# Optimization experiments

Measured on AMD Instinct MI355X. Metric: run time of the kernel, lower is better.

Reference implementation:

```python
import jax, jax.numpy as jnp
import numpy as np

# dims: D=embed_dim (= number of experts), H=heads, P=image patches, Q=query embeddings, B=batch
D, H, N, P, B, Q = 256, 8, 256, 1024, 1, 64
HD = D // H
EPS = 1e-5


def _ln(x, g, b):
    m = x.mean(-1, keepdims=True)
    v = x.var(-1, keepdims=True)
    return (x - m) / jnp.sqrt(v + EPS) * g + b


def _mha(q_x, kv_x, Wqkv, bqkv, Wo, bo):
    # standard torch nn.MultiheadAttention (batch_first, eval mode)
    Wq, Wk, Wv = jnp.split(Wqkv, 3, axis=0)
    bq, bk, bv = jnp.split(bqkv, 3, axis=0)
    q = q_x @ Wq.T + bq
    k = kv_x @ Wk.T + bk
    v = kv_x @ Wv.T + bv
    Bq, S, _ = q.shape
    Sk = k.shape[1]
    qh = q.reshape(Bq, S, H, HD)
    kh = k.reshape(Bq, Sk, H, HD)
    vh = v.reshape(Bq, Sk, H, HD)
    att = jax.nn.softmax(jnp.einsum('bqhd,bkhd->bhqk', qh, kh) / np.sqrt(HD).astype(np.float32), axis=-1)
    ctx = jnp.einsum('bhqk,bkhd->bqhd', att, vh).reshape(Bq, S, D)
    return ctx @ Wo.T + bo


def setup_inputs() -> dict:
    key = jax.random.key(0)
    ks = jax.random.split(key, 12)
    s = 0.02  # weight init scale
    return {
        'image_patches': jax.random.normal(ks[0], (B, P, D), jnp.float32),
        'expert_tokens': jax.random.normal(ks[1], (B, N, D), jnp.float32),
        'query_embeddings': jax.random.normal(ks[2], (B, Q, D), jnp.float32),
        'Wqkv_experts': jax.random.normal(ks[3], (N, 3 * D, D), jnp.float32) * s,
        'bqkv_experts': jnp.zeros((N, 3 * D), jnp.float32),
        'Wo_experts': jax.random.normal(ks[4], (N, D, D), jnp.float32) * s,
        'bo_experts': jnp.zeros((N, D), jnp.float32),
        'Wqkv_q': jax.random.normal(ks[5], (3 * D, D), jnp.float32) * s,
        'bqkv_q': jnp.zeros((3 * D,), jnp.float32),
        'Wo_q': jax.random.normal(ks[6], (D, D), jnp.float32) * s,
        'bo_q': jnp.zeros((D,), jnp.float32),
        'Wqkv_s': jax.random.normal(ks[7], (3 * D, D), jnp.float32) * s,
        'bqkv_s': jnp.zeros((3 * D,), jnp.float32),
        'Wo_s': jax.random.normal(ks[8], (D, D), jnp.float32) * s,
        'bo_s': jnp.zeros((D,), jnp.float32),
        'W1': jax.random.normal(ks[9], (4 * D, D), jnp.float32) * s,
        'b1': jnp.zeros((4 * D,), jnp.float32),
        'W2': jax.random.normal(ks[10], (D, 4 * D), jnp.float32) * s,
        'b2': jnp.zeros((D,), jnp.float32),
        'ln1_g': jnp.ones((D,), jnp.float32), 'ln1_b': jnp.zeros((D,), jnp.float32),
        'ln2_g': jnp.ones((D,), jnp.float32), 'ln2_b': jnp.zeros((D,), jnp.float32),
        'ln3_g': jnp.ones((D,), jnp.float32), 'ln3_b': jnp.zeros((D,), jnp.float32),
    }


def reference(image_patches, expert_tokens, query_embeddings,
              Wqkv_experts, bqkv_experts, Wo_experts, bo_experts,
              Wqkv_q, bqkv_q, Wo_q, bo_q,
              Wqkv_s, bqkv_s, Wo_s, bo_s,
              W1, b1, W2, b2,
              ln1_g, ln1_b, ln2_g, ln2_b, ln3_g, ln3_b):
    # --- per-expert cross attention (the embed_dim separate MHA calls, fused/batched) ---
    Wq, Wk, Wv = jnp.split(Wqkv_experts, 3, axis=1)   # each [N, D, D]
    bq, bk, bv = jnp.split(bqkv_experts, 3, axis=1)   # each [N, D]
    q = jnp.einsum('bnd,ned->bne', expert_tokens, Wq) + bq                       # [B,N,D]
    K = jnp.einsum('bpd,ned->bnpe', image_patches, Wk) + bk[None, :, None, :]    # [B,N,P,D]
    V = jnp.einsum('bpd,ned->bnpe', image_patches, Wv) + bv[None, :, None, :]    # [B,N,P,D]
    qh = q.reshape(B, N, H, HD)
    Kh = K.reshape(B, N, P, H, HD)
    Vh = V.reshape(B, N, P, H, HD)
    att = jax.nn.softmax(jnp.einsum('bnhd,bnphd->bnhp', qh, Kh) / np.sqrt(HD).astype(np.float32), axis=-1)
    image_attention_weights = att.mean(axis=2)        # [B,N,P] head-averaged, torch default
    ctx = jnp.einsum('bnhp,bnphd->bnhd', att, Vh).reshape(B, N, D)
    attended_image = jnp.einsum('bnd,ned->bne', ctx, Wo_experts) + bo_experts    # [B,N,D]
    attended_image = _ln(attended_image + expert_tokens, ln1_g, ln1_b)
    # --- query cross attention ---
    attended_query = _mha(attended_image, query_embeddings, Wqkv_q, bqkv_q, Wo_q, bo_q)
    attended_query = _ln(attended_query + attended_image, ln2_g, ln2_b)
    # --- FFN (no residual in original) ---
    expert_refined = jax.nn.relu(attended_query @ W1.T + b1) @ W2.T + b2
    # --- expert self attention + residual + norm ---
    sa = _mha(expert_refined, expert_refined, Wqkv_s, bqkv_s, Wo_s, bo_s)
    expert_features = _ln(sa + expert_refined, ln3_g, ln3_b)
    return expert_features, image_attention_weights
```

## Files before the change

kernel.cpp:

```cpp
#include <hip/hip_runtime.h>

#define DD 256
#define NH 8
#define NP 1024
#define NQ 64
#define SCALE 0.17677669529663687f

typedef float f32x4v __attribute__((ext_vector_type(4)));
typedef __bf16 bfv8 __attribute__((ext_vector_type(8)));

union BF8 { bfv8 v; unsigned short u16[8]; uint4 q; };

__device__ __forceinline__ float wred_sum(float p) {
  #pragma unroll
  for (int m = 32; m; m >>= 1) p += __shfl_xor(p, m);
  return p;
}
__device__ __forceinline__ float wred_max(float p) {
  #pragma unroll
  for (int m = 32; m; m >>= 1) p = fmaxf(p, __shfl_xor(p, m));
  return p;
}
__device__ __forceinline__ float red8(float p) {
  p += __shfl_xor(p, 1);
  p += __shfl_xor(p, 2);
  p += __shfl_xor(p, 4);
  return p;
}
__device__ __forceinline__ float red16(float p) {
  p += __shfl_xor(p, 1);
  p += __shfl_xor(p, 2);
  p += __shfl_xor(p, 4);
  p += __shfl_xor(p, 8);
  return p;
}
__device__ __forceinline__ float dot4(float4 a, float4 b) {
  return a.x*b.x + a.y*b.y + a.z*b.z + a.w*b.w;
}
__device__ __forceinline__ unsigned short f2b(float f) {
  unsigned int u = __float_as_uint(f);
  u += 0x7fffu + ((u >> 16) & 1u);
  return (unsigned short)(u >> 16);
}
__device__ __forceinline__ BF8 cvt8(float4 a, float4 b) {
  BF8 r;
  r.u16[0]=f2b(a.x); r.u16[1]=f2b(a.y); r.u16[2]=f2b(a.z); r.u16[3]=f2b(a.w);
  r.u16[4]=f2b(b.x); r.u16[5]=f2b(b.y); r.u16[6]=f2b(b.z); r.u16[7]=f2b(b.w);
  return r;
}
__device__ __forceinline__ f32x4v mfma16(BF8 a, BF8 b, f32x4v c) {
  return __builtin_amdgcn_mfma_f32_16x16x32_bf16(a.v, b.v, c, 0, 0, 0);
}
__device__ __forceinline__ float2 b2f2(unsigned int u) {
  return make_float2(__uint_as_float(u << 16), __uint_as_float(u & 0xffff0000u));
}
__device__ __forceinline__ float dotb8(uint4 w, float4 x0, float4 x1) {
  float2 p0 = b2f2(w.x), p1 = b2f2(w.y), p2 = b2f2(w.z), p3 = b2f2(w.w);
  return p0.x*x0.x + p0.y*x0.y + p1.x*x0.z + p1.y*x0.w
       + p2.x*x1.x + p2.y*x1.y + p3.x*x1.z + p3.y*x1.w;
}

__device__ __forceinline__ void preload8(const float* x, int lane, float4* xf) {
  const int o = (lane & 7) * 4;
  #pragma unroll
  for (int cc = 0; cc < 8; ++cc) xf[cc] = *(const float4*)&x[cc*32 + o];
}
__device__ __forceinline__ void pass16(const float* __restrict__ W, int ldk,
                                       int r0, int lane, const float4* xf,
                                       float* outA, float* outB) {
  const float* baseA = W + (size_t)(r0 + (lane >> 3))*ldk + (lane & 7)*4;
  const float* baseB = baseA + (size_t)8*ldk;
  float4 wa[8], wb[8];
  #pragma unroll
  for (int cc = 0; cc < 8; ++cc) wa[cc] = *(const float4*)&baseA[cc*32];
  #pragma unroll
  for (int cc = 0; cc < 8; ++cc) wb[cc] = *(const float4*)&baseB[cc*32];
  float a = 0.f, b = 0.f;
  #pragma unroll
  for (int cc = 0; cc < 8; ++cc) { a += dot4(wa[cc], xf[cc]); b += dot4(wb[cc], xf[cc]); }
  *outA = red8(a); *outB = red8(b);
}
__device__ __forceinline__ void preload8b(const float* x, int lane, float4* xf) {
  const int o = (lane & 7) * 8;
  #pragma unroll
  for (int cc = 0; cc < 4; ++cc) {
    xf[2*cc]   = *(const float4*)&x[cc*64 + o];
    xf[2*cc+1] = *(const float4*)&x[cc*64 + o + 4];
  }
}
__device__ __forceinline__ void pass16b(const unsigned short* __restrict__ W, int ldk,
                                        int r0, int lane, const float4* xf,
                                        float* outA, float* outB) {
  const unsigned short* baseA = W + (size_t)(r0 + (lane >> 3))*ldk + (lane & 7)*8;
  const unsigned short* baseB = baseA + (size_t)8*ldk;
  uint4 wa[4], wb[4];
  #pragma unroll
  for (int cc = 0; cc < 4; ++cc) wa[cc] = *(const uint4*)&baseA[cc*64];
  #pragma unroll
  for (int cc = 0; cc < 4; ++cc) wb[cc] = *(const uint4*)&baseB[cc*64];
  float a = 0.f, b = 0.f;
  #pragma unroll
  for (int cc = 0; cc < 4; ++cc) {
    a += dotb8(wa[cc], xf[2*cc], xf[2*cc+1]);
    b += dotb8(wb[cc], xf[2*cc], xf[2*cc+1]);
  }
  *outA = red8(a); *outB = red8(b);
}

__device__ __forceinline__ void layernorm_store(const float* buf, float* outp,
                                                const float* g, const float* b,
                                                float* red, int tid, int wid, int lane)
{
  __syncthreads();
  if (wid == 0) {
    float s = buf[lane] + buf[lane+64] + buf[lane+128] + buf[lane+192];
    s = wred_sum(s);
    if (!lane) red[0] = s * (1.f/256.f);
  }
  __syncthreads();
  float mn = red[0];
  if (wid == 0) {
    float d0 = buf[lane]-mn, d1 = buf[lane+64]-mn, d2 = buf[lane+128]-mn, d3 = buf[lane+192]-mn;
    float s = d0*d0 + d1*d1 + d2*d2 + d3*d3;
    s = wred_sum(s);
    if (!lane) red[1] = rsqrtf(s * (1.f/256.f) + 1e-5f);
  }
  __syncthreads();
  if (tid < 256) outp[tid] = (buf[tid] - mn) * red[1] * g[tid] + b[tid];
}

__device__ __forceinline__ void stage8(const float* __restrict__ Wrow0, float* stf, int lane) {
  #pragma unroll
  for (int r = 0; r < 8; ++r)
    __builtin_amdgcn_global_load_lds(
      (const __attribute__((address_space(1))) unsigned int*)(Wrow0 + (size_t)r*DD + lane*4),
      (__attribute__((address_space(3))) unsigned int*)(stf + r*258), 16, 0, 0);
}
#define WAITV0() { asm volatile("s_waitcnt vmcnt(0)" ::: "memory"); __builtin_amdgcn_sched_barrier(0); }
#define ENDIT()  { asm volatile("s_waitcnt lgkmcnt(0)" ::: "memory"); __builtin_amdgcn_sched_barrier(0); }

__device__ __forceinline__ float rowdot4(const float* stf, int row, int j, const float4* xq) {
  float a = 0.f;
  #pragma unroll
  for (int cc = 0; cc < 4; ++cc) {
    float4 wv = *(const float4*)&stf[row*258 + cc*64 + j*4];
    a += dot4(wv, xq[cc]);
  }
  return red16(a);
}

__global__ __launch_bounds__(256)
void k_pre(const float* __restrict__ patches, uint4* __restrict__ pTB,
           uint4* __restrict__ patchesB,
           const float* __restrict__ qe, const float* __restrict__ Wqkv_q,
           const float* __restrict__ bqkv_q, float* __restrict__ kvq,
           const float* __restrict__ Wo_q, const float* __restrict__ W1,
           const float* __restrict__ W2, const float* __restrict__ Wqkv_s,
           unsigned short* __restrict__ wsB)
{
  const int b = blockIdx.x, tid = threadIdx.x;
  if (b < 128) {
    const int T = b*4 + (tid >> 6), l = tid & 63;
    const int kt = T >> 6, nt = T & 63;
    const int row = nt*16 + (l & 15), col = kt*32 + (l >> 4)*8;
    float4 a = *(const float4*)&patches[(size_t)row*DD + col];
    float4 c = *(const float4*)&patches[(size_t)row*DD + col + 4];
    pTB[(size_t)T*64 + l] = cvt8(a, c).q;
  } else if (b < 256) {
    const int T = (b - 128)*4 + (tid >> 6), l = tid & 63;
    const int kt = T >> 4, nt = T & 15;
    const int col = nt*16 + (l & 15), p0 = kt*32 + (l >> 4)*8;
    float v[8];
    #pragma unroll
    for (int j = 0; j < 8; ++j) v[j] = patches[(size_t)(p0 + j)*DD + col];
    BF8 r;
    #pragma unroll
    for (int j = 0; j < 8; ++j) r.u16[j] = f2b(v[j]);
    patchesB[(size_t)T*64 + l] = r.q;
  } else if (b < 320) {
    __shared__ float x[DD], kvrow[512];
    const int j = b - 256, w = tid >> 6, lane = tid & 63;
    if (tid < DD) x[tid] = qe[j*DD + tid];
    __syncthreads();
    float4 xf[8]; preload8(x, lane, xf);
    #pragma unroll
    for (int g = 0; g < 8; ++g) {
      int r0 = w*128 + g*16;
      float a, bb;
      pass16(Wqkv_q + (size_t)DD*DD, DD, r0, lane, xf, &a, &bb);
      int rA = r0 + (lane >> 3);
      if ((lane & 7) == 0) {
        kvrow[rA]   = a  + bqkv_q[DD + rA];
        kvrow[rA+8] = bb + bqkv_q[DD + rA + 8];
      }
    }
    __syncthreads();
    kvq[(size_t)j*512 + tid]       = kvrow[tid];
    kvq[(size_t)j*512 + 256 + tid] = kvrow[256 + tid];
  } else {
    const int gid = (b - 320)*256 + tid;
    const float* src;
    size_t dof;
    if      (gid < 8192)  { src = Wqkv_q + (size_t)gid*8;           dof = (size_t)gid*8; }
    else if (gid < 16384) { src = Wo_q   + (size_t)(gid-8192)*8;    dof = 65536  + (size_t)(gid-8192)*8; }
    else if (gid < 49152) { src = W1     + (size_t)(gid-16384)*8;   dof = 131072 + (size_t)(gid-16384)*8; }
    else if (gid < 81920) { src = W2     + (size_t)(gid-49152)*8;   dof = 393216 + (size_t)(gid-49152)*8; }
    else                  { src = Wqkv_s + (size_t)(gid-81920)*8;   dof = 655360 + (size_t)(gid-81920)*8; }
    float4 a = *(const float4*)&src[0];
    float4 c = *(const float4*)&src[4];
    *(uint4*)&wsB[dof] = cvt8(a, c).q;
  }
}

__global__ __launch_bounds__(512)
void k_front(const float* __restrict__ et_g,
             const float* __restrict__ Wqkv_e, const float* __restrict__ bqkv_e,
             const float* __restrict__ Wo_e, const float* __restrict__ bo_e,
             const uint4* __restrict__ pTB, const uint4* __restrict__ patchesB,
             const float* __restrict__ ln1g, const float* __restrict__ ln1b,
             float* __restrict__ aln_g, float* __restrict__ iaw)
{
  const int n = blockIdx.x, tid = threadIdx.x, w = tid >> 6, lane = tid & 63;
  __shared__ float stageF[8*8*258];
  __shared__ float attS[NH][NP];
  __shared__ __align__(16) uint4 attB[16][128];
  __shared__ float tS[16][260];
  __shared__ float uS[NH][DD];
  __shared__ float xL[DD], qL[DD], ctxL[DD], resS[DD], red2[2];

  const float* Wn = Wqkv_e + (size_t)n*(3*DD*DD);
  const float* bn = bqkv_e + (size_t)n*(3*DD);
  float* stf = &stageF[w*2064];
  const int j16 = lane & 15, g16 = lane >> 4;

  if (tid < DD) xL[tid] = et_g[(size_t)n*DD + tid];
  __syncthreads();

  {
    float4 xq[4];
    #pragma unroll
    for (int cc = 0; cc < 4; ++cc) xq[cc] = *(const float4*)&xL[j16*4 + cc*64];
    #pragma unroll
    for (int grp = 0; grp < 4; ++grp) {
      stage8(Wn + (size_t)(w*32 + grp*8)*DD, stf, lane);
      WAITV0();
      float a0 = rowdot4(stf, g16,     j16, xq);
      float a1 = rowdot4(stf, 4 + g16, j16, xq);
      if (j16 == 0) {
        qL[w*32 + grp*8 + g16]     = a0;
        qL[w*32 + grp*8 + 4 + g16] = a1;
      }
      ENDIT();
    }
    if (lane < 32) qL[w*32 + lane] += bn[w*32 + lane];
  }

  {
    const float* Wk = Wn + (size_t)DD*DD + (size_t)w*32*DD;
    float4 acc = make_float4(0.f, 0.f, 0.f, 0.f);
    #pragma unroll
    for (int grp = 0; grp < 4; ++grp) {
      stage8(Wk + (size_t)grp*8*DD, stf, lane);
      WAITV0();
      #pragma unroll
      for (int r = 0; r < 8; ++r) {
        float qs = qL[w*32 + grp*8 + r];
        float4 wv = *(const float4*)&stf[r*258 + lane*4];
        acc.x += qs*wv.x; acc.y += qs*wv.y; acc.z += qs*wv.z; acc.w += qs*wv.w;
      }
      ENDIT();
    }
    *(float4*)&tS[w][4*lane] = acc;
  }
  __syncthreads();

  BF8 afr[8];
  {
    const int rr = lane & 15, ko = (lane >> 4)*8;
    #pragma unroll
    for (int kt = 0; kt < 8; ++kt) {
      float4 a = *(const float4*)&tS[rr][kt*32 + ko];
      float4 c = *(const float4*)&tS[rr][kt*32 + ko + 4];
      afr[kt] = cvt8(a, c);
    }
  }
  {
    #pragma unroll
    for (int t8 = 0; t8 < 8; ++t8) {
      const int nt = w*8 + t8;
      f32x4v acc = {0.f, 0.f, 0.f, 0.f};
      #pragma unroll
      for (int kt = 0; kt < 8; ++kt) {
        BF8 bb; bb.q = pTB[(size_t)(kt*64 + nt)*64 + lane];
        acc = mfma16(afr[kt], bb, acc);
      }
      if (lane < 32) {
        const int r0 = (lane >> 4)*4, cc = nt*16 + (lane & 15);
        #pragma unroll
        for (int i = 0; i < 4; ++i) attS[r0 + i][cc] = acc[i];
      }
    }
  }
  __syncthreads();

  {
    const int h = w;
    float v[16];
    #pragma unroll
    for (int k = 0; k < 16; ++k) v[k] = attS[h][k*64 + lane] * SCALE;
    float mx = v[0];
    #pragma unroll
    for (int k = 1; k < 16; ++k) mx = fmaxf(mx, v[k]);
    mx = wred_max(mx);
    float sum = 0.f;
    #pragma unroll
    for (int k = 0; k < 16; ++k) { v[k] = __expf(v[k] - mx); sum += v[k]; }
    sum = wred_sum(sum);
    float rinv = 1.f / sum;
    #pragma unroll
    for (int k = 0; k < 16; ++k) attS[h][k*64 + lane] = v[k] * rinv;
  }
  __syncthreads();

  #pragma unroll
  for (int rep = 0; rep < 2; ++rep) {
    int p = rep*512 + tid;
    float s = 0.f;
    #pragma unroll
    for (int h = 0; h < NH; ++h) s += attS[h][p];
    iaw[(size_t)n*NP + p] = s * 0.125f;
  }
  #pragma unroll
  for (int rep = 0; rep < 2; ++rep) {
    int C = rep*512 + tid;
    int row = C >> 7, c = C & 127;
    float4 a = *(const float4*)&attS[row][c*8];
    float4 b = *(const float4*)&attS[row][c*8 + 4];
    int swz = (c & ~7) | ((c ^ row) & 7);
    attB[row][swz] = cvt8(a, b).q;
  }
  __syncthreads();

  {
    const int nt0 = 2*w, nt1 = 2*w + 1;
    f32x4v acc0 = {0.f,0.f,0.f,0.f}, acc1 = {0.f,0.f,0.f,0.f};
    const int rr = lane & 15, cq = lane >> 4;
    #pragma unroll 8
    for (int kt = 0; kt < 32; ++kt) {
      int cc = kt*4 + cq;
      int swz = (cc & ~7) | ((cc ^ rr) & 7);
      BF8 a;  a.q  = attB[rr][swz];
      BF8 b0; b0.q = patchesB[(size_t)(kt*16 + nt0)*64 + lane];
      BF8 b1; b1.q = patchesB[(size_t)(kt*16 + nt1)*64 + lane];
      acc0 = mfma16(a, b0, acc0);
      acc1 = mfma16(a, b1, acc1);
    }
    if (lane < 32) {
      const int r0 = (lane >> 4)*4;
      #pragma unroll
      for (int i = 0; i < 4; ++i) {
        uS[r0+i][nt0*16 + (lane & 15)] = acc0[i];
        uS[r0+i][nt1*16 + (lane & 15)] = acc1[i];
      }
    }
  }
  __syncthreads();

  {
    float4 xq[4];
    #pragma unroll
    for (int cc = 0; cc < 4; ++cc) xq[cc] = *(const float4*)&uS[w][j16*4 + cc*64];
    const float* Wv = Wn + (size_t)2*DD*DD;
    #pragma unroll
    for (int grp = 0; grp < 4; ++grp) {
      stage8(Wv + (size_t)(w*32 + grp*8)*DD, stf, lane);
      WAITV0();
      float a0 = rowdot4(stf, g16,     j16, xq);
      float a1 = rowdot4(stf, 4 + g16, j16, xq);
      if (j16 == 0) {
        int r = w*32 + grp*8 + g16;
        ctxL[r]     = a0 + bn[2*DD + r];
        ctxL[r + 4] = a1 + bn[2*DD + r + 4];
      }
      ENDIT();
    }
  }
  __syncthreads();

  {
    float4 xq[4];
    #pragma unroll
    for (int cc = 0; cc < 4; ++cc) xq[cc] = *(const float4*)&ctxL[j16*4 + cc*64];
    const float* Won = Wo_e + (size_t)n*DD*DD;
    #pragma unroll
    for (int grp = 0; grp < 4; ++grp) {
      stage8(Won + (size_t)(w*32 + grp*8)*DD, stf, lane);
      WAITV0();
      float a0 = rowdot4(stf, g16,     j16, xq);
      float a1 = rowdot4(stf, 4 + g16, j16, xq);
      if (j16 == 0) {
        int r = w*32 + grp*8 + g16;
        resS[r]     = a0 + bo_e[(size_t)n*DD + r]     + xL[r];
        resS[r + 4] = a1 + bo_e[(size_t)n*DD + r + 4] + xL[r + 4];
      }
      ENDIT();
    }
  }
  layernorm_store(resS, aln_g + (size_t)n*DD, ln1g, ln1b, red2, tid, w, lane);
}

__global__ __launch_bounds__(1024)
void k_mid(const float* __restrict__ aln, const float* __restrict__ kvq,
           const unsigned short* __restrict__ wsB,
           const float* __restrict__ bqkv_q, const float* __restrict__ bo_q,
           const float* __restrict__ b1, const float* __restrict__ b2,
           const float* __restrict__ bqkv_s,
           const float* __restrict__ ln2g, const float* __restrict__ ln2b,
           float* __restrict__ er_g, float* __restrict__ qkvs_g)
{
  const int n = blockIdx.x, tid = threadIdx.x, w = tid >> 6, lane = tid & 63;
  __shared__ float xL[DD], qL[DD], ctxL[DD], resS[DD], attq[NH][NQ], red2[2];
  __shared__ float hb[1024], qrow[768];
  const unsigned short* WqB  = wsB;
  const unsigned short* WoqB = wsB + 65536;
  const unsigned short* W1B  = wsB + 131072;
  const unsigned short* W2B  = wsB + 393216;
  const unsigned short* WsB  = wsB + 655360;

  if (tid < DD) xL[tid] = aln[(size_t)n*DD + tid];
  __syncthreads();

  {
    float4 xf[8]; preload8b(xL, lane, xf);
    float a, b;
    pass16b(WqB, DD, w*16, lane, xf, &a, &b);
    int rA = w*16 + (lane >> 3);
    if ((lane & 7) == 0) { qL[rA] = a + bqkv_q[rA]; qL[rA+8] = b + bqkv_q[rA+8]; }
  }
  __syncthreads();
  if (w < 8) {
    const int h = w, j = lane;
    float4 q4[8];
    #pragma unroll
    for (int m = 0; m < 8; ++m) q4[m] = *(const float4*)&qL[h*32 + 4*m];
    const float* kj = kvq + (size_t)j*512 + h*32;
    float s = 0.f;
    #pragma unroll
    for (int m = 0; m < 8; ++m) s += dot4(*(const float4*)&kj[4*m], q4[m]);
    s *= SCALE;
    float mx = wred_max(s);
    float p = __expf(s - mx);
    float sum = wred_sum(p);
    attq[h][j] = p / sum;
  }
  __syncthreads();
  if (tid < DD) {
    const int rr = tid, h = rr >> 5;
    float acc = 0.f;
    #pragma unroll 4
    for (int j4 = 0; j4 < 16; ++j4) {
      float4 a4 = *(const float4*)&attq[h][j4*4];
      acc += a4.x * kvq[(size_t)(j4*4+0)*512 + DD + rr]
           + a4.y * kvq[(size_t)(j4*4+1)*512 + DD + rr]
           + a4.z * kvq[(size_t)(j4*4+2)*512 + DD + rr]
           + a4.w * kvq[(size_t)(j4*4+3)*512 + DD + rr];
    }
    ctxL[rr] = acc;
  }
  __syncthreads();
  {
    float4 xf[8]; preload8b(ctxL, lane, xf);
    float a, b;
    pass16b(WoqB, DD, w*16, lane, xf, &a, &b);
    int rA = w*16 + (lane >> 3);
    if ((lane & 7) == 0) { resS[rA] = a + bo_q[rA] + xL[rA]; resS[rA+8] = b + bo_q[rA+8] + xL[rA+8]; }
  }
  layernorm_store(resS, xL, ln2g, ln2b, red2, tid, w, lane);
  __syncthreads();

  {
    float4 xf[8]; preload8b(xL, lane, xf);
    #pragma unroll
    for (int g = 0; g < 4; ++g) {
      int r0 = w*64 + g*16;
      float a, b;
      pass16b(W1B, DD, r0, lane, xf, &a, &b);
      int rA = r0 + (lane >> 3);
      if ((lane & 7) == 0) { hb[rA] = fmaxf(a + b1[rA], 0.f); hb[rA+8] = fmaxf(b + b1[rA+8], 0.f); }
    }
  }
  __syncthreads();
  {
    float accA = 0.f, accB = 0.f;
    #pragma unroll
    for (int kc = 0; kc < 4; ++kc) {
      float4 xh[8]; preload8b(hb + kc*256, lane, xh);
      float a, b;
      pass16b(W2B + kc*256, 1024, w*16, lane, xh, &a, &b);
      accA += a; accB += b;
    }
    int rA = w*16 + (lane >> 3);
    if ((lane & 7) == 0) { qL[rA] = accA + b2[rA]; qL[rA+8] = accB + b2[rA+8]; }
  }
  __syncthreads();
  {
    float4 xf[8]; preload8b(qL, lane, xf);
    #pragma unroll
    for (int g = 0; g < 3; ++g) {
      int r0 = w*48 + g*16;
      float a, b;
      pass16b(WsB, DD, r0, lane, xf, &a, &b);
      int rA = r0 + (lane >> 3);
      if ((lane & 7) == 0) { qrow[rA] = a + bqkv_s[rA]; qrow[rA+8] = b + bqkv_s[rA+8]; }
    }
  }
  __syncthreads();
  if (tid < 768) qkvs_g[(size_t)n*768 + tid] = qrow[tid];
  if (tid < DD)  er_g[(size_t)n*DD + tid]   = qL[tid];
}

__global__ __launch_bounds__(1024)
void k_sa(const float* __restrict__ er, const float* __restrict__ qkvs,
          const float* __restrict__ Wo_s, const float* __restrict__ bo_s,
          const float* __restrict__ ln3g, const float* __restrict__ ln3b,
          float* __restrict__ ef)
{
  const int i = blockIdx.x, tid = threadIdx.x, w = tid >> 6, lane = tid & 63;
  __shared__ float x[DD], attl[NH][256], ctxp[4][DD], resS[DD], red2[2];
  if (tid < DD) x[tid] = er[(size_t)i*DD + tid];
  {
    const int h = w & 7, kh = w >> 3;
    float4 q4[8];
    #pragma unroll
    for (int m = 0; m < 8; ++m) q4[m] = *(const float4*)&qkvs[(size_t)i*768 + h*32 + 4*m];
    #pragma unroll
    for (int rep = 0; rep < 2; ++rep) {
      int j = kh*128 + rep*64 + lane;
      const float* kj = qkvs + (size_t)j*768 + DD + h*32;
      float4 k4[8];
      #pragma unroll
      for (int m = 0; m < 8; ++m) k4[m] = *(const float4*)&kj[4*m];
      float s = 0.f;
      #pragma unroll
      for (int m = 0; m < 8; ++m) s += dot4(k4[m], q4[m]);
      attl[h][j] = s * SCALE;
    }
  }
  __syncthreads();
  if (w < 8) {
    const int h = w;
    float v0 = attl[h][lane], v1 = attl[h][lane+64], v2 = attl[h][lane+128], v3 = attl[h][lane+192];
    float mx = wred_max(fmaxf(fmaxf(v0,v1), fmaxf(v2,v3)));
    float e0 = __expf(v0-mx), e1 = __expf(v1-mx), e2 = __expf(v2-mx), e3 = __expf(v3-mx);
    float sum = wred_sum(e0+e1+e2+e3);
    float r = 1.f/sum;
    attl[h][lane] = e0*r; attl[h][lane+64] = e1*r; attl[h][lane+128] = e2*r; attl[h][lane+192] = e3*r;
  }
  __syncthreads();
  {
    const int rr = tid & 255, qtr = tid >> 8, h = rr >> 5;
    float acc = 0.f;
    #pragma unroll 4
    for (int j4 = qtr*16; j4 < qtr*16 + 16; ++j4) {
      float4 a4 = *(const float4*)&attl[h][j4*4];
      acc += a4.x * qkvs[(size_t)(j4*4+0)*768 + 512 + rr]
           + a4.y * qkvs[(size_t)(j4*4+1)*768 + 512 + rr]
           + a4.z * qkvs[(size_t)(j4*4+2)*768 + 512 + rr]
           + a4.w * qkvs[(size_t)(j4*4+3)*768 + 512 + rr];
    }
    ctxp[qtr][rr] = acc;
  }
  __syncthreads();
  {
    float4 xf[8];
    const int o = (lane & 7)*4;
    #pragma unroll
    for (int cc = 0; cc < 8; ++cc) {
      float4 a = *(const float4*)&ctxp[0][cc*32 + o];
      float4 b = *(const float4*)&ctxp[1][cc*32 + o];
      float4 c = *(const float4*)&ctxp[2][cc*32 + o];
      float4 d = *(const float4*)&ctxp[3][cc*32 + o];
      xf[cc] = make_float4(a.x+b.x+c.x+d.x, a.y+b.y+c.y+d.y,
                           a.z+b.z+c.z+d.z, a.w+b.w+c.w+d.w);
    }
    float a, b;
    pass16(Wo_s, DD, w*16, lane, xf, &a, &b);
    int rA = w*16 + (lane >> 3);
    if ((lane & 7) == 0) { resS[rA] = a + bo_s[rA] + x[rA]; resS[rA+8] = b + bo_s[rA+8] + x[rA+8]; }
  }
  layernorm_store(resS, ef + (size_t)i*DD, ln3g, ln3b, red2, tid, w, lane);
}

extern "C" void kernel_launch(void* const* d_in, const int* in_sizes, int n_in,
                              void* d_out, int out_size, void* d_ws, size_t ws_size,
                              hipStream_t stream) {
  const float* patches = (const float*)d_in[0];
  const float* et      = (const float*)d_in[1];
  const float* qe      = (const float*)d_in[2];
  const float* Wqkv_e  = (const float*)d_in[3];
  const float* bqkv_e  = (const float*)d_in[4];
  const float* Wo_e    = (const float*)d_in[5];
  const float* bo_e    = (const float*)d_in[6];
  const float* Wqkv_q  = (const float*)d_in[7];
  const float* bqkv_q  = (const float*)d_in[8];
  const float* Wo_q    = (const float*)d_in[9];
  const float* bo_q    = (const float*)d_in[10];
  const float* Wqkv_s  = (const float*)d_in[11];
  const float* bqkv_s  = (const float*)d_in[12];
  const float* Wo_s    = (const float*)d_in[13];
  const float* bo_s    = (const float*)d_in[14];
  const float* W1      = (const float*)d_in[15];
  const float* b1      = (const float*)d_in[16];
  const float* W2      = (const float*)d_in[17];
  const float* b2      = (const float*)d_in[18];
  const float* ln1g = (const float*)d_in[19]; const float* ln1b = (const float*)d_in[20];
  const float* ln2g = (const float*)d_in[21]; const float* ln2b = (const float*)d_in[22];
  const float* ln3g = (const float*)d_in[23]; const float* ln3b = (const float*)d_in[24];

  float* ef  = (float*)d_out;
  float* iaw = (float*)d_out + 65536;

  float* ws           = (float*)d_ws;
  uint4* pTB          = (uint4*)ws;
  uint4* patchesB     = (uint4*)(ws + 131072);
  float* kvq          = ws + 262144;
  float* aln          = ws + 294912;
  float* er           = ws + 360448;
  float* qkvs         = ws + 425984;
  unsigned short* wsB = (unsigned short*)(ws + 622592);

  k_pre<<<736, 256, 0, stream>>>(patches, pTB, patchesB, qe, Wqkv_q, bqkv_q, kvq,
                                 Wo_q, W1, W2, Wqkv_s, wsB);
  k_front<<<256, 512, 0, stream>>>(et, Wqkv_e, bqkv_e, Wo_e, bo_e,
                                   pTB, patchesB, ln1g, ln1b, aln, iaw);
  k_mid<<<256, 1024, 0, stream>>>(aln, kvq, wsB, bqkv_q, bo_q, b1, b2, bqkv_s,
                                  ln2g, ln2b, er, qkvs);
  k_sa<<<256, 1024, 0, stream>>>(er, qkvs, Wo_s, bo_s, ln3g, ln3b, ef);
}
```

Baseline: 140.3 us.

## Split expert front kernel into three stages with double-buffered weight staging

The monolithic per-expert front kernel becomes three kernels: q/t projection, patch attention, and V/output projection, with intermediates passed through workspace buffers. The weight-streaming loops now double-buffer LDS staging and wait on vmcnt(8), so the next 8-row chunk loads while the current one is consumed. LayerNorm1 moves into the tail kernel. This trades extra launches and global round-trips of intermediates for better per-kernel occupancy and overlap of the dominant weight reads.

Measured after the change: 153.2 us. +9.2%, slower.

```diff
diff --git a/kernel.cpp b/kernel.cpp
--- a/kernel.cpp
+++ b/kernel.cpp
@@ -136,8 +136,8 @@
       (const __attribute__((address_space(1))) unsigned int*)(Wrow0 + (size_t)r*DD + lane*4),
       (__attribute__((address_space(3))) unsigned int*)(stf + r*258), 16, 0, 0);
 }
-#define WAITV0() { asm volatile("s_waitcnt vmcnt(0)" ::: "memory"); __builtin_amdgcn_sched_barrier(0); }
-#define ENDIT()  { asm volatile("s_waitcnt lgkmcnt(0)" ::: "memory"); __builtin_amdgcn_sched_barrier(0); }
+#define WAIT8() { asm volatile("s_waitcnt vmcnt(8)" ::: "memory"); __builtin_amdgcn_sched_barrier(0); }
+#define WAIT0() { asm volatile("s_waitcnt vmcnt(0)" ::: "memory"); __builtin_amdgcn_sched_barrier(0); }
 
 __device__ __forceinline__ float rowdot4(const float* stf, int row, int j, const float4* xq) {
   float a = 0.f;
@@ -213,65 +213,73 @@
 }
 
 __global__ __launch_bounds__(512)
-void k_front(const float* __restrict__ et_g,
-             const float* __restrict__ Wqkv_e, const float* __restrict__ bqkv_e,
-             const float* __restrict__ Wo_e, const float* __restrict__ bo_e,
-             const uint4* __restrict__ pTB, const uint4* __restrict__ patchesB,
-             const float* __restrict__ ln1g, const float* __restrict__ ln1b,
-             float* __restrict__ aln_g, float* __restrict__ iaw)
+void k_qt(const float* __restrict__ et_g, const float* __restrict__ Wqkv_e,
+          const float* __restrict__ bqkv_e, float* __restrict__ t_ws)
 {
   const int n = blockIdx.x, tid = threadIdx.x, w = tid >> 6, lane = tid & 63;
-  __shared__ float stageF[8*8*258];
+  __shared__ float stageF[8][2][2064];
+  __shared__ float xL[DD], qL[DD];
+  const float* Wn = Wqkv_e + (size_t)n*(3*DD*DD);
+  const float* bn = bqkv_e + (size_t)n*(3*DD);
+  float* st0 = &stageF[w][0][0];
+  float* st1 = &stageF[w][1][0];
+  const int j16 = lane & 15, g16 = lane >> 4;
+
+  if (tid < DD) xL[tid] = et_g[(size_t)n*DD + tid];
+  __syncthreads();
+
+  float4 xq[4];
+  #pragma unroll
+  for (int cc = 0; cc < 4; ++cc) xq[cc] = *(const float4*)&xL[j16*4 + cc*64];
+
+  const float* Wq = Wn + (size_t)w*32*DD;
+  const float* Wk = Wn + (size_t)DD*DD + (size_t)w*32*DD;
+  float4 tacc = make_float4(0.f, 0.f, 0.f, 0.f);
+
+  stage8(Wq, st0, lane);
+  #pragma unroll
+  for (int g = 0; g < 8; ++g) {
+    float* cur = (g & 1) ? st1 : st0;
+    float* nxt = (g & 1) ? st0 : st1;
+    if (g < 7) {
+      const float* src = (g + 1 < 4) ? (Wq + (size_t)(g+1)*8*DD) : (Wk + (size_t)(g+1-4)*8*DD);
+      stage8(src, nxt, lane);
+      WAIT8();
+    } else {
+      WAIT0();
+    }
+    if (g < 4) {
+      float a0 = rowdot4(cur, g16,     j16, xq);
+      float a1 = rowdot4(cur, 4 + g16, j16, xq);
+      if (j16 == 0) {
+        int r = w*32 + g*8 + g16;
+        qL[r]     = a0 + bn[r];
+        qL[r + 4] = a1 + bn[r + 4];
+      }
+    } else {
+      #pragma unroll
+      for (int r = 0; r < 8; ++r) {
+        float qs = qL[w*32 + (g - 4)*8 + r];
+        float4 wv = *(const float4*)&cur[r*258 + lane*4];
+        tacc.x += qs*wv.x; tacc.y += qs*wv.y; tacc.z += qs*wv.z; tacc.w += qs*wv.w;
+      }
+    }
+  }
+  *(float4*)&t_ws[(size_t)n*2048 + w*256 + 4*lane] = tacc;
+}
+
+__global__ __launch_bounds__(512)
+void k_mid1(const float* __restrict__ t_ws,
+            const uint4* __restrict__ pTB, const uint4* __restrict__ patchesB,
+            float* __restrict__ u_ws, float* __restrict__ iaw)
+{
+  const int n = blockIdx.x, tid = threadIdx.x, w = tid >> 6, lane = tid & 63;
   __shared__ float attS[NH][NP];
   __shared__ __align__(16) uint4 attB[16][128];
   __shared__ float tS[16][260];
   __shared__ float uS[NH][DD];
-  __shared__ float xL[DD], qL[DD], ctxL[DD], resS[DD], red2[2];
-
-  const float* Wn = Wqkv_e + (size_t)n*(3*DD*DD);
-  const float* bn = bqkv_e + (size_t)n*(3*DD);
-  float* stf = &stageF[w*2064];
-  const int j16 = lane & 15, g16 = lane >> 4;
-
-  if (tid < DD) xL[tid] = et_g[(size_t)n*DD + tid];
-  __syncthreads();
-
-  {
-    float4 xq[4];
-    #pragma unroll
-    for (int cc = 0; cc < 4; ++cc) xq[cc] = *(const float4*)&xL[j16*4 + cc*64];
-    #pragma unroll
-    for (int grp = 0; grp < 4; ++grp) {
-      stage8(Wn + (size_t)(w*32 + grp*8)*DD, stf, lane);
-      WAITV0();
-      float a0 = rowdot4(stf, g16,     j16, xq);
-      float a1 = rowdot4(stf, 4 + g16, j16, xq);
-      if (j16 == 0) {
-        qL[w*32 + grp*8 + g16]     = a0;
-        qL[w*32 + grp*8 + 4 + g16] = a1;
-      }
-      ENDIT();
-    }
-    if (lane < 32) qL[w*32 + lane] += bn[w*32 + lane];
-  }
-
-  {
-    const float* Wk = Wn + (size_t)DD*DD + (size_t)w*32*DD;
-    float4 acc = make_float4(0.f, 0.f, 0.f, 0.f);
-    #pragma unroll
-    for (int grp = 0; grp < 4; ++grp) {
-      stage8(Wk + (size_t)grp*8*DD, stf, lane);
-      WAITV0();
-      #pragma unroll
-      for (int r = 0; r < 8; ++r) {
-        float qs = qL[w*32 + grp*8 + r];
-        float4 wv = *(const float4*)&stf[r*258 + lane*4];
-        acc.x += qs*wv.x; acc.y += qs*wv.y; acc.z += qs*wv.z; acc.w += qs*wv.w;
-      }
-      ENDIT();
-    }
-    *(float4*)&tS[w][4*lane] = acc;
-  }
+
+  for (int idx = tid; idx < 2048; idx += 512) tS[idx >> 8][idx & 255] = t_ws[(size_t)n*2048 + idx];
   __syncthreads();
 
   BF8 afr[8];
@@ -302,7 +310,6 @@
     }
   }
   __syncthreads();
-
   {
     const int h = w;
     float v[16];
@@ -321,7 +328,6 @@
     for (int k = 0; k < 16; ++k) attS[h][k*64 + lane] = v[k] * rinv;
   }
   __syncthreads();
-
   #pragma unroll
   for (int rep = 0; rep < 2; ++rep) {
     int p = rep*512 + tid;
@@ -340,7 +346,6 @@
     attB[row][swz] = cvt8(a, b).q;
   }
   __syncthreads();
-
   {
     const int nt0 = 2*w, nt1 = 2*w + 1;
     f32x4v acc0 = {0.f,0.f,0.f,0.f}, acc1 = {0.f,0.f,0.f,0.f};
@@ -365,58 +370,79 @@
     }
   }
   __syncthreads();
+  for (int idx = tid; idx < 2048; idx += 512) u_ws[(size_t)n*2048 + idx] = (&uS[0][0])[idx];
+}
+
+__global__ __launch_bounds__(512)
+void k_ctxout(const float* __restrict__ u_ws, const float* __restrict__ et_g,
+              const float* __restrict__ Wqkv_e, const float* __restrict__ bqkv_e,
+              const float* __restrict__ Wo_e, const float* __restrict__ bo_e,
+              float* __restrict__ res_ws)
+{
+  const int n = blockIdx.x, tid = threadIdx.x, w = tid >> 6, lane = tid & 63;
+  __shared__ float stageF[8][2][2064];
+  __shared__ float ctxL[DD];
+  const float* Wn = Wqkv_e + (size_t)n*(3*DD*DD);
+  const float* bn = bqkv_e + (size_t)n*(3*DD);
+  float* st0 = &stageF[w][0][0];
+  float* st1 = &stageF[w][1][0];
+  const int j16 = lane & 15, g16 = lane >> 4;
 
   {
     float4 xq[4];
     #pragma unroll
-    for (int cc = 0; cc < 4; ++cc) xq[cc] = *(const float4*)&uS[w][j16*4 + cc*64];
-    const float* Wv = Wn + (size_t)2*DD*DD;
-    #pragma unroll
-    for (int grp = 0; grp < 4; ++grp) {
-      stage8(Wv + (size_t)(w*32 + grp*8)*DD, stf, lane);
-      WAITV0();
-      float a0 = rowdot4(stf, g16,     j16, xq);
-      float a1 = rowdot4(stf, 4 + g16, j16, xq);
+    for (int cc = 0; cc < 4; ++cc)
+      xq[cc] = *(const float4*)&u_ws[(size_t)n*2048 + w*256 + j16*4 + cc*64];
+    const float* Wv = Wn + (size_t)2*DD*DD + (size_t)w*32*DD;
+    stage8(Wv, st0, lane);
+    #pragma unroll
+    for (int g = 0; g < 4; ++g) {
+      float* cur = (g & 1) ? st1 : st0;
+      float* nxt = (g & 1) ? st0 : st1;
+      if (g < 3) { stage8(Wv + (size_t)(g+1)*8*DD, nxt, lane); WAIT8(); }
+      else       { WAIT0(); }
+      float a0 = rowdot4(cur, g16,     j16, xq);
+      float a1 = rowdot4(cur, 4 + g16, j16, xq);
       if (j16 == 0) {
-        int r = w*32 + grp*8 + g16;
+        int r = w*32 + g*8 + g16;
         ctxL[r]     = a0 + bn[2*DD + r];
         ctxL[r + 4] = a1 + bn[2*DD + r + 4];
       }
-      ENDIT();
-    }
-  }
-  __syncthreads();
-
+    }
+  }
+  __syncthreads();
   {
     float4 xq[4];
     #pragma unroll
     for (int cc = 0; cc < 4; ++cc) xq[cc] = *(const float4*)&ctxL[j16*4 + cc*64];
-    const float* Won = Wo_e + (size_t)n*DD*DD;
-    #pragma unroll
-    for (int grp = 0; grp < 4; ++grp) {
-      stage8(Won + (size_t)(w*32 + grp*8)*DD, stf, lane);
-      WAITV0();
-      float a0 = rowdot4(stf, g16,     j16, xq);
-      float a1 = rowdot4(stf, 4 + g16, j16, xq);
+    const float* Won = Wo_e + (size_t)n*DD*DD + (size_t)w*32*DD;
+    stage8(Won, st0, lane);
+    #pragma unroll
+    for (int g = 0; g < 4; ++g) {
+      float* cur = (g & 1) ? st1 : st0;
+      float* nxt = (g & 1) ? st0 : st1;
+      if (g < 3) { stage8(Won + (size_t)(g+1)*8*DD, nxt, lane); WAIT8(); }
+      else       { WAIT0(); }
+      float a0 = rowdot4(cur, g16,     j16, xq);
+      float a1 = rowdot4(cur, 4 + g16, j16, xq);
       if (j16 == 0) {
-        int r = w*32 + grp*8 + g16;
-        resS[r]     = a0 + bo_e[(size_t)n*DD + r]     + xL[r];
-        resS[r + 4] = a1 + bo_e[(size_t)n*DD + r + 4] + xL[r + 4];
-      }
-      ENDIT();
-    }
-  }
-  layernorm_store(resS, aln_g + (size_t)n*DD, ln1g, ln1b, red2, tid, w, lane);
+        int r = w*32 + g*8 + g16;
+        res_ws[(size_t)n*DD + r]     = a0 + bo_e[(size_t)n*DD + r]     + et_g[(size_t)n*DD + r];
+        res_ws[(size_t)n*DD + r + 4] = a1 + bo_e[(size_t)n*DD + r + 4] + et_g[(size_t)n*DD + r + 4];
+      }
+    }
+  }
 }
 
 __global__ __launch_bounds__(1024)
-void k_mid(const float* __restrict__ aln, const float* __restrict__ kvq,
-           const unsigned short* __restrict__ wsB,
-           const float* __restrict__ bqkv_q, const float* __restrict__ bo_q,
-           const float* __restrict__ b1, const float* __restrict__ b2,
-           const float* __restrict__ bqkv_s,
-           const float* __restrict__ ln2g, const float* __restrict__ ln2b,
-           float* __restrict__ er_g, float* __restrict__ qkvs_g)
+void k_tail(const float* __restrict__ res_ws, const float* __restrict__ kvq,
+            const unsigned short* __restrict__ wsB,
+            const float* __restrict__ bqkv_q, const float* __restrict__ bo_q,
+            const float* __restrict__ b1, const float* __restrict__ b2,
+            const float* __restrict__ bqkv_s,
+            const float* __restrict__ ln1g, const float* __restrict__ ln1b,
+            const float* __restrict__ ln2g, const float* __restrict__ ln2b,
+            float* __restrict__ er_g, float* __restrict__ qkvs_g)
 {
   const int n = blockIdx.x, tid = threadIdx.x, w = tid >> 6, lane = tid & 63;
   __shared__ float xL[DD], qL[DD], ctxL[DD], resS[DD], attq[NH][NQ], red2[2];
@@ -427,7 +453,8 @@
   const unsigned short* W2B  = wsB + 393216;
   const unsigned short* WsB  = wsB + 655360;
 
-  if (tid < DD) xL[tid] = aln[(size_t)n*DD + tid];
+  if (tid < DD) resS[tid] = res_ws[(size_t)n*DD + tid];
+  layernorm_store(resS, xL, ln1g, ln1b, red2, tid, w, lane);
   __syncthreads();
 
   {
@@ -624,16 +651,19 @@
   uint4* pTB          = (uint4*)ws;
   uint4* patchesB     = (uint4*)(ws + 131072);
   float* kvq          = ws + 262144;
-  float* aln          = ws + 294912;
-  float* er           = ws + 360448;
-  float* qkvs         = ws + 425984;
-  unsigned short* wsB = (unsigned short*)(ws + 622592);
+  float* t_ws         = ws + 294912;
+  float* u_ws         = ws + 819200;
+  float* res_ws       = ws + 1343488;
+  float* er           = ws + 1409024;
+  float* qkvs         = ws + 1474560;
+  unsigned short* wsB = (unsigned short*)(ws + 1671168);
 
   k_pre<<<736, 256, 0, stream>>>(patches, pTB, patchesB, qe, Wqkv_q, bqkv_q, kvq,
                                  Wo_q, W1, W2, Wqkv_s, wsB);
-  k_front<<<256, 512, 0, stream>>>(et, Wqkv_e, bqkv_e, Wo_e, bo_e,
-                                   pTB, patchesB, ln1g, ln1b, aln, iaw);
-  k_mid<<<256, 1024, 0, stream>>>(aln, kvq, wsB, bqkv_q, bo_q, b1, b2, bqkv_s,
-                                  ln2g, ln2b, er, qkvs);
+  k_qt<<<256, 512, 0, stream>>>(et, Wqkv_e, bqkv_e, t_ws);
+  k_mid1<<<256, 512, 0, stream>>>(t_ws, pTB, patchesB, u_ws, iaw);
+  k_ctxout<<<256, 512, 0, stream>>>(u_ws, et, Wqkv_e, bqkv_e, Wo_e, bo_e, res_ws);
+  k_tail<<<256, 1024, 0, stream>>>(res_ws, kvq, wsB, bqkv_q, bo_q, b1, b2, bqkv_s,
+                                   ln1g, ln1b, ln2g, ln2b, er, qkvs);
   k_sa<<<256, 1024, 0, stream>>>(er, qkvs, Wo_s, bo_s, ln3g, ln3b, ef);
 }
```
